# Kernel tuning notes

Hardware: AMD Instinct MI355X
Metric: run time of the kernel (lower is better)

The kernel has to match this reference:

```python
import jax, jax.numpy as jnp
import numpy as np

B, S, HID, NH = 2, 2048, 1024, 16
HD = HID // NH
BASE = 10000.0


def _rope_tables(seq_len, head_dim):
    i = jnp.arange(0, head_dim, 2, dtype=jnp.float32)
    theta = BASE ** (-i / head_dim)
    pos = jnp.arange(seq_len, dtype=jnp.float32)
    m_theta = jnp.outer(pos, theta)  # [S, HD/2]
    cos = jnp.repeat(jnp.cos(m_theta), 2, axis=1)  # [S, HD]
    sin = jnp.repeat(jnp.sin(m_theta), 2, axis=1)
    return cos, sin


def _apply_rope(x, cos, sin):
    # x: [B, NH, S, HD]; interleaved rotation: (-x1, x0, -x3, x2, ...)
    x_even = x[..., 0::2]
    x_odd = x[..., 1::2]
    inv_x = jnp.stack((-x_odd, x_even), axis=-1).reshape(x.shape)
    return x * cos[None, None] + inv_x * sin[None, None]


def setup_inputs() -> dict:
    key = jax.random.key(0)
    ks = jax.random.split(key, 7)
    q = jax.random.normal(ks[0], (B, S, HID), dtype=jnp.float32)
    k = jax.random.normal(ks[1], (B, S, HID), dtype=jnp.float32)
    v = jax.random.normal(ks[2], (B, S, HID), dtype=jnp.float32)
    scale = 1.0 / np.sqrt(HID)
    Wq = jax.random.normal(ks[3], (HID, HID), dtype=jnp.float32) * scale
    Wk = jax.random.normal(ks[4], (HID, HID), dtype=jnp.float32) * scale
    Wv = jax.random.normal(ks[5], (HID, HID), dtype=jnp.float32) * scale
    Wo = jax.random.normal(ks[6], (HID, HID), dtype=jnp.float32) * scale
    mask = jnp.triu(jnp.ones((S, S), dtype=bool), k=1)[None, None]  # causal, True = masked
    return {"q": q, "k": k, "v": v, "mask": mask,
            "Wq": Wq, "Wk": Wk, "Wv": Wv, "Wo": Wo}


def reference(q, k, v, mask, Wq, Wk, Wv, Wo):
    cos, sin = _rope_tables(S, HD)
    # Linear (torch stores weight as [out, in]; y = x @ W.T)
    qh = (q @ Wq.T).reshape(B, S, NH, HD).transpose(0, 2, 1, 3)
    kh = (k @ Wk.T).reshape(B, S, NH, HD).transpose(0, 2, 1, 3)
    vh = (v @ Wv.T).reshape(B, S, NH, HD).transpose(0, 2, 1, 3)
    qh = _apply_rope(qh, cos, sin)
    kh = _apply_rope(kh, cos, sin)
    scores = jnp.einsum("bhqd,bhkd->bhqk", qh, kh) / np.sqrt(HD)
    neg_min = jnp.finfo(jnp.float32).min
    scores = jnp.where(mask, neg_min, scores)
    attn = jax.nn.softmax(scores, axis=-1)
    out = jnp.einsum("bhqk,bhkd->bhqd", attn, vh)  # [B,NH,S,HD]
    out = out.transpose(0, 2, 1, 3).reshape(B, S, HID)
    return out @ Wo.T
```

## Files before the change

### kernel.cpp

```cpp
#include <hip/hip_runtime.h>

#define S_LEN 2048
#define HIDN  1024
#define NHEAD 16
#define HDIM  64
#define MROWS 4096
#define KDIM  1024
#define NDIM  1024

typedef __attribute__((ext_vector_type(8))) short bf16x8;
typedef __attribute__((ext_vector_type(4))) float f32x4;

static __device__ __forceinline__ ushort f2bf(float f) {
    unsigned int u = __float_as_uint(f);
    u = (u + 0x7fffu + ((u >> 16) & 1u)) >> 16;
    return (ushort)u;
}

static __device__ __forceinline__ void gload16(const ushort* g, ushort* l) {
    __builtin_amdgcn_global_load_lds(
        (const __attribute__((address_space(1))) unsigned int*)g,
        (__attribute__((address_space(3))) unsigned int*)l, 16, 0, 0);
}

__global__ __launch_bounds__(256) void prep_kernel(
    const float* __restrict__ q, const float* __restrict__ k,
    const float* __restrict__ v, const float* __restrict__ Wq,
    const float* __restrict__ Wk, const float* __restrict__ Wv,
    const float* __restrict__ Wo,
    ushort* __restrict__ qb, ushort* __restrict__ kb, ushort* __restrict__ vb,
    ushort* __restrict__ Wqb, ushort* __restrict__ Wkb, ushort* __restrict__ Wvb,
    ushort* __restrict__ Wob,
    float* __restrict__ rc, float* __restrict__ rs)
{
    const long Q4 = (long)MROWS * KDIM / 4;
    const long W4 = (long)NDIM * KDIM / 4;
    if (blockIdx.x < 16384) {
        long i = (long)blockIdx.x * 256 + threadIdx.x;
        const float* src; ushort* dst; long off;
        if (i < Q4)          { src = q; dst = qb; off = i; }
        else if (i < 2 * Q4) { src = k; dst = kb; off = i - Q4; }
        else if (i < 3 * Q4) { src = v; dst = vb; off = i - 2 * Q4; }
        else {
            long t = i - 3 * Q4;
            int wsel = (int)(t >> 18);
            off = t & (W4 - 1);
            src = (wsel == 0) ? Wq : (wsel == 1) ? Wk : (wsel == 2) ? Wv : Wo;
            dst = (wsel == 0) ? Wqb : (wsel == 1) ? Wkb : (wsel == 2) ? Wvb : Wob;
        }
        float4 vv = ((const float4*)src)[off];
        ushort4 o;
        o.x = f2bf(vv.x); o.y = f2bf(vv.y); o.z = f2bf(vv.z); o.w = f2bf(vv.w);
        ((ushort4*)dst)[off] = o;
    } else {
        int idx = (blockIdx.x - 16384) * 256 + threadIdx.x;
        int s  = idx >> 5;
        int jp = idx & 31;
        float theta = expf(-(float)(2 * jp) * (9.210340371976184f / 64.0f));
        float ang = (float)s * theta;
        float sv, cv;
        sincosf(ang, &sv, &cv);
        rc[idx] = cv;
        rs[idx] = sv;
    }
}

static __device__ __forceinline__ void gemm_mainloop(
    const ushort* __restrict__ A, const ushort* __restrict__ W,
    ushort* As, ushort* Bs, f32x4 (&acc)[2][4],
    int m0, int n0, int tid)
{
    const int lane = tid & 63, wid = tid >> 6;
    const int wm = wid & 1, wn = wid >> 1;
    const int quad = lane >> 4, l15 = lane & 15;

    for (int k0 = 0; k0 < KDIM; k0 += 64) {
        __syncthreads();
#pragma unroll
        for (int rr = 0; rr < 2; ++rr) {
            int sidx = tid + rr * 256;
            int row = sidx >> 3;
            int g = (sidx & 7) ^ (row & 7);
            gload16(A + (size_t)(m0 + row) * KDIM + k0 + g * 8, As + sidx * 8);
        }
#pragma unroll
        for (int rr = 0; rr < 4; ++rr) {
            int sidx = tid + rr * 256;
            int row = sidx >> 3;
            int g = (sidx & 7) ^ (row & 7);
            gload16(W + (size_t)(n0 + row) * KDIM + k0 + g * 8, Bs + sidx * 8);
        }
        __syncthreads();

#pragma unroll
        for (int ks = 0; ks < 2; ++ks) {
            bf16x8 af[2], bfr[4];
#pragma unroll
            for (int i = 0; i < 2; ++i) {
                int row = wm * 32 + i * 16 + l15;
                int gg = ((ks << 2) | quad) ^ (row & 7);
                af[i] = *(const bf16x8*)&As[row * 64 + gg * 8];
            }
#pragma unroll
            for (int j = 0; j < 4; ++j) {
                int row = wn * 64 + j * 16 + l15;
                int gg = ((ks << 2) | quad) ^ (row & 7);
                bfr[j] = *(const bf16x8*)&Bs[row * 64 + gg * 8];
            }
#pragma unroll
            for (int i = 0; i < 2; ++i)
#pragma unroll
                for (int j = 0; j < 4; ++j)
                    acc[i][j] = __builtin_amdgcn_mfma_f32_16x16x32_bf16(
                        af[i], bfr[j], acc[i][j], 0, 0, 0);
        }
    }
}

__global__ __launch_bounds__(256) void gemm_qkv(
    const ushort* __restrict__ qb, const ushort* __restrict__ kb,
    const ushort* __restrict__ vb,
    const ushort* __restrict__ Wqb, const ushort* __restrict__ Wkb,
    const ushort* __restrict__ Wvb,
    ushort* __restrict__ Qh, ushort* __restrict__ Kh, ushort* __restrict__ Vt,
    const float* __restrict__ rc, const float* __restrict__ rs)
{
    __shared__ __align__(16) ushort As[64 * 64];
    __shared__ __align__(16) ushort Bs[128 * 64];

    const int tid = threadIdx.x;
    const int lane = tid & 63, wid = tid >> 6;
    const int wm = wid & 1, wn = wid >> 1;
    const int quad = lane >> 4, l15 = lane & 15;
    const int z = blockIdx.z;

    const ushort* A; const ushort* W; int m0, n0;
    if (z == 2) {
        int flat = blockIdx.y * 8 + blockIdx.x;
        m0 = (flat >> 5) * 64;
        n0 = (flat & 31) * 128;
        A = Wvb; W = vb;
    } else {
        m0 = blockIdx.y * 64; n0 = blockIdx.x * 128;
        A = (z == 0) ? qb : kb;
        W = (z == 0) ? Wqb : Wkb;
    }

    f32x4 acc[2][4];
#pragma unroll
    for (int i = 0; i < 2; ++i)
#pragma unroll
        for (int j = 0; j < 4; ++j) acc[i][j] = 0.0f;

    gemm_mainloop(A, W, As, Bs, acc, m0, n0, tid);

    if (z != 2) {
        ushort* out = (z == 0) ? Qh : Kh;
        const float scale = (z == 0) ? 0.18033688011112042f : 1.0f;
#pragma unroll
        for (int i = 0; i < 2; ++i)
#pragma unroll
            for (int j = 0; j < 4; ++j)
#pragma unroll
                for (int r = 0; r < 4; ++r) {
                    int m = m0 + wm * 32 + i * 16 + quad * 4 + r;
                    int n = n0 + wn * 64 + j * 16 + l15;
                    float v = acc[i][j][r];
                    int b = m >> 11, s = m & (S_LEN - 1);
                    int h = n >> 6, d = n & 63;
                    int pidx = s * 32 + (d >> 1);
                    float cv = rc[pidx], sv = rs[pidx];
                    float partner = __shfl_xor(v, 1);
                    v = (d & 1) ? (v * cv + partner * sv)
                                : (v * cv - partner * sv);
                    out[((size_t)((b * NHEAD + h) * S_LEN + s)) * HDIM + d] =
                        f2bf(v * scale);
                }
    } else {
#pragma unroll
        for (int i = 0; i < 2; ++i)
#pragma unroll
            for (int j = 0; j < 4; ++j)
#pragma unroll
                for (int r = 0; r < 4; ++r) {
                    int m = m0 + wm * 32 + i * 16 + quad * 4 + r;
                    int n = n0 + wn * 64 + j * 16 + l15;
                    int h = m >> 6, d = m & 63;
                    int b = n >> 11, s = n & (S_LEN - 1);
                    Vt[((size_t)((b * NHEAD + h) * HDIM + d)) * S_LEN + s] =
                        f2bf(acc[i][j][r]);
                }
    }
}

__global__ __launch_bounds__(256) void gemm_out(
    const ushort* __restrict__ A, const ushort* __restrict__ W,
    float* __restrict__ out)
{
    __shared__ __align__(16) ushort As[64 * 64];
    __shared__ __align__(16) ushort Bs[128 * 64];

    const int tid = threadIdx.x;
    const int lane = tid & 63, wid = tid >> 6;
    const int wm = wid & 1, wn = wid >> 1;
    const int quad = lane >> 4, l15 = lane & 15;
    const int m0 = blockIdx.y * 64, n0 = blockIdx.x * 128;

    f32x4 acc[2][4];
#pragma unroll
    for (int i = 0; i < 2; ++i)
#pragma unroll
        for (int j = 0; j < 4; ++j) acc[i][j] = 0.0f;

    gemm_mainloop(A, W, As, Bs, acc, m0, n0, tid);

#pragma unroll
    for (int i = 0; i < 2; ++i)
#pragma unroll
        for (int j = 0; j < 4; ++j)
#pragma unroll
            for (int r = 0; r < 4; ++r) {
                int m = m0 + wm * 32 + i * 16 + quad * 4 + r;
                int n = n0 + wn * 64 + j * 16 + l15;
                out[(size_t)m * NDIM + n] = acc[i][j][r];
            }
}

__global__ __launch_bounds__(256) void attn_mfma(
    const ushort* __restrict__ Qh, const ushort* __restrict__ Kh,
    const ushort* __restrict__ Vt, ushort* __restrict__ AO)
{
    __shared__ __align__(16) ushort Ks[64 * 64];
    __shared__ __align__(16) ushort Vs[64 * 64];
    __shared__ __align__(16) ushort Ps[64 * 72];

    const int tid = threadIdx.x;
    const int lane = tid & 63, w = tid >> 6;
    const int quad = lane >> 4, l15 = lane & 15;
    const int id = blockIdx.x;
    const int b = id >> 9, h = (id >> 5) & 15, xr = id & 31;
    const int qt = b ? (31 - xr) : xr;
    const int q0 = qt * 64;
    const size_t hoff = (size_t)(b * NHEAD + h) * S_LEN * HDIM;

    bf16x8 qf[2];
#pragma unroll
    for (int ks = 0; ks < 2; ++ks)
        qf[ks] = *(const bf16x8*)(Qh + hoff +
            (size_t)(q0 + w * 16 + l15) * HDIM + ks * 32 + quad * 8);

    bf16x8 ones;
#pragma unroll
    for (int i = 0; i < 8; ++i) ones[i] = (short)0x3F80;

    f32x4 Oa[4];
    f32x4 Lacc = 0.0f;
#pragma unroll
    for (int j = 0; j < 4; ++j) Oa[j] = 0.0f;

    const int rowq = q0 + w * 16 + quad * 4;

    for (int kt = 0; kt <= qt; ++kt) {
        const int k0 = kt * 64;
        const bool diag = (kt == qt);
        __syncthreads();
#pragma unroll
        for (int rr = 0; rr < 2; ++rr) {
            int sidx = tid + rr * 256;
            int row = sidx >> 3;
            int g = (sidx & 7) ^ (row & 7);
            gload16(Kh + hoff + (size_t)(k0 + row) * HDIM + g * 8, Ks + sidx * 8);
            gload16(Vt + hoff + (size_t)row * S_LEN + k0 + g * 8, Vs + sidx * 8);
        }
        __syncthreads();

        f32x4 Sa[4];
#pragma unroll
        for (int j = 0; j < 4; ++j) Sa[j] = 0.0f;
#pragma unroll
        for (int ks = 0; ks < 2; ++ks) {
            const int p = ((ks << 2) | quad) ^ (l15 & 7);
            bf16x8 kf[4];
#pragma unroll
            for (int j = 0; j < 4; ++j)
                kf[j] = *(const bf16x8*)&Ks[(j * 16 + l15) * 64 + p * 8];
#pragma unroll
            for (int j = 0; j < 4; ++j)
                Sa[j] = __builtin_amdgcn_mfma_f32_16x16x32_bf16(qf[ks], kf[j],
                                                                Sa[j], 0, 0, 0);
        }

#pragma unroll
        for (int j = 0; j < 4; ++j) {
#pragma unroll
            for (int r = 0; r < 4; ++r) {
                float p = exp2f(Sa[j][r]);
                if (diag) {
                    int key = k0 + j * 16 + l15;
                    if (key > rowq + r) p = 0.f;
                }
                Ps[(w * 16 + quad * 4 + r) * 72 + j * 16 + l15] =
                    (ushort)(__float_as_uint(p) >> 16);
            }
        }

#pragma unroll
        for (int ks = 0; ks < 2; ++ks) {
            const int p = ((ks << 2) | quad) ^ (l15 & 7);
            bf16x8 pf = *(const bf16x8*)&Ps[(w * 16 + l15) * 72 + ks * 32 + quad * 8];
            bf16x8 vf[4];
#pragma unroll
            for (int j = 0; j < 4; ++j)
                vf[j] = *(const bf16x8*)&Vs[(j * 16 + l15) * 64 + p * 8];
#pragma unroll
            for (int j = 0; j < 4; ++j)
                Oa[j] = __builtin_amdgcn_mfma_f32_16x16x32_bf16(pf, vf[j],
                                                                Oa[j], 0, 0, 0);
            Lacc = __builtin_amdgcn_mfma_f32_16x16x32_bf16(pf, ones, Lacc, 0, 0, 0);
        }
    }

#pragma unroll
    for (int r = 0; r < 4; ++r) {
        float inv = 1.0f / Lacc[r];
        int srow = rowq + r;
#pragma unroll
        for (int j = 0; j < 4; ++j) {
            int d = j * 16 + l15;
            AO[((size_t)(b * S_LEN + srow)) * HIDN + h * HDIM + d] =
                f2bf(Oa[j][r] * inv);
        }
    }
}

extern "C" void kernel_launch(void* const* d_in, const int* in_sizes, int n_in,
                              void* d_out, int out_size, void* d_ws, size_t ws_size,
                              hipStream_t stream) {
    const float* qf  = (const float*)d_in[0];
    const float* kf  = (const float*)d_in[1];
    const float* vf  = (const float*)d_in[2];
    const float* Wqf = (const float*)d_in[4];
    const float* Wkf = (const float*)d_in[5];
    const float* Wvf = (const float*)d_in[6];
    const float* Wof = (const float*)d_in[7];
    float* out = (float*)d_out;

    char* wsp = (char*)d_ws;
    float* rc = (float*)wsp;            wsp += 65536 * 4;
    float* rs = (float*)wsp;            wsp += 65536 * 4;
    ushort* qb  = (ushort*)wsp;         wsp += (size_t)MROWS * KDIM * 2;
    ushort* kb  = (ushort*)wsp;         wsp += (size_t)MROWS * KDIM * 2;
    ushort* vb  = (ushort*)wsp;         wsp += (size_t)MROWS * KDIM * 2;
    ushort* Wqb = (ushort*)wsp;         wsp += (size_t)NDIM * KDIM * 2;
    ushort* Wkb = (ushort*)wsp;         wsp += (size_t)NDIM * KDIM * 2;
    ushort* Wvb = (ushort*)wsp;         wsp += (size_t)NDIM * KDIM * 2;
    ushort* Wob = (ushort*)wsp;         wsp += (size_t)NDIM * KDIM * 2;
    ushort* Qh  = (ushort*)wsp;         wsp += (size_t)MROWS * HIDN * 2;
    ushort* Kh  = (ushort*)wsp;         wsp += (size_t)MROWS * HIDN * 2;
    ushort* Vt  = (ushort*)wsp;         wsp += (size_t)MROWS * HIDN * 2;
    ushort* AO  = (ushort*)wsp;

    prep_kernel<<<16640, 256, 0, stream>>>(qf, kf, vf, Wqf, Wkf, Wvf, Wof,
                                           qb, kb, vb, Wqb, Wkb, Wvb, Wob, rc, rs);

    gemm_qkv<<<dim3(8, 64, 3), 256, 0, stream>>>(
        qb, kb, vb, Wqb, Wkb, Wvb, Qh, Kh, Vt, rc, rs);

    attn_mfma<<<1024, 256, 0, stream>>>(Qh, Kh, Vt, AO);

    gemm_out<<<dim3(8, 64), 256, 0, stream>>>(AO, Wob, out);
}
```

Baseline: 225.8 us.

## Split causal attention across blocks for load balance and add combine kernel

```diff
diff --git a/kernel.cpp b/kernel.cpp
--- a/kernel.cpp
+++ b/kernel.cpp
@@ -15,6 +15,9 @@
     unsigned int u = __float_as_uint(f);
     u = (u + 0x7fffu + ((u >> 16) & 1u)) >> 16;
     return (ushort)u;
+}
+static __device__ __forceinline__ float bf2f(ushort u) {
+    return __uint_as_float(((unsigned int)u) << 16);
 }
 
 static __device__ __forceinline__ void gload16(const ushort* g, ushort* l) {
@@ -136,12 +139,11 @@
 
     const ushort* A; const ushort* W; int m0, n0;
     if (z == 2) {
-        int flat = blockIdx.y * 8 + blockIdx.x;
-        m0 = (flat >> 5) * 64;
-        n0 = (flat & 31) * 128;
+        m0 = ((int)blockIdx.y * 2 + ((int)blockIdx.x >> 5)) * 64;
+        n0 = ((int)blockIdx.x & 31) * 128;
         A = Wvb; W = vb;
     } else {
-        m0 = blockIdx.y * 64; n0 = blockIdx.x * 128;
+        m0 = blockIdx.x * 64; n0 = blockIdx.y * 128;
         A = (z == 0) ? qb : kb;
         W = (z == 0) ? Wqb : Wkb;
     }
@@ -204,7 +206,7 @@
     const int lane = tid & 63, wid = tid >> 6;
     const int wm = wid & 1, wn = wid >> 1;
     const int quad = lane >> 4, l15 = lane & 15;
-    const int m0 = blockIdx.y * 64, n0 = blockIdx.x * 128;
+    const int m0 = blockIdx.x * 64, n0 = blockIdx.y * 128;
 
     f32x4 acc[2][4];
 #pragma unroll
@@ -228,7 +230,9 @@
 
 __global__ __launch_bounds__(256) void attn_mfma(
     const ushort* __restrict__ Qh, const ushort* __restrict__ Kh,
-    const ushort* __restrict__ Vt, ushort* __restrict__ AO)
+    const ushort* __restrict__ Vt,
+    ushort* __restrict__ O0, ushort* __restrict__ O1,
+    float* __restrict__ L0, float* __restrict__ L1)
 {
     __shared__ __align__(16) ushort Ks[64 * 64];
     __shared__ __align__(16) ushort Vs[64 * 64];
@@ -238,99 +242,125 @@
     const int lane = tid & 63, w = tid >> 6;
     const int quad = lane >> 4, l15 = lane & 15;
     const int id = blockIdx.x;
-    const int b = id >> 9, h = (id >> 5) & 15, xr = id & 31;
-    const int qt = b ? (31 - xr) : xr;
-    const int q0 = qt * 64;
+    const int h = id & 15, y = (id >> 4) & 31, b = id >> 9;
     const size_t hoff = (size_t)(b * NHEAD + h) * S_LEN * HDIM;
 
-    bf16x8 qf[2];
-#pragma unroll
-    for (int ks = 0; ks < 2; ++ks)
-        qf[ks] = *(const bf16x8*)(Qh + hoff +
-            (size_t)(q0 + w * 16 + l15) * HDIM + ks * 32 + quad * 8);
-
     bf16x8 ones;
 #pragma unroll
     for (int i = 0; i < 8; ++i) ones[i] = (short)0x3F80;
 
-    f32x4 Oa[4];
-    f32x4 Lacc = 0.0f;
-#pragma unroll
-    for (int j = 0; j < 4; ++j) Oa[j] = 0.0f;
-
-    const int rowq = q0 + w * 16 + quad * 4;
-
-    for (int kt = 0; kt <= qt; ++kt) {
-        const int k0 = kt * 64;
-        const bool diag = (kt == qt);
-        __syncthreads();
-#pragma unroll
-        for (int rr = 0; rr < 2; ++rr) {
-            int sidx = tid + rr * 256;
-            int row = sidx >> 3;
-            int g = (sidx & 7) ^ (row & 7);
-            gload16(Kh + hoff + (size_t)(k0 + row) * HDIM + g * 8, Ks + sidx * 8);
-            gload16(Vt + hoff + (size_t)row * S_LEN + k0 + g * 8, Vs + sidx * 8);
-        }
-        __syncthreads();
-
-        f32x4 Sa[4];
-#pragma unroll
-        for (int j = 0; j < 4; ++j) Sa[j] = 0.0f;
-#pragma unroll
-        for (int ks = 0; ks < 2; ++ks) {
-            const int p = ((ks << 2) | quad) ^ (l15 & 7);
-            bf16x8 kf[4];
+#pragma unroll
+    for (int seg = 0; seg < 2; ++seg) {
+        const int qt = seg ? (31 - y) : y;
+        const int lo = seg ? ((33 - y) >> 1) : 0;
+        const int hi = seg ? (32 - y) : ((y + 2) >> 1);
+        const int q0 = qt * 64;
+
+        bf16x8 qf[2];
+#pragma unroll
+        for (int ks = 0; ks < 2; ++ks)
+            qf[ks] = *(const bf16x8*)(Qh + hoff +
+                (size_t)(q0 + w * 16 + l15) * HDIM + ks * 32 + quad * 8);
+
+        f32x4 Oa[4];
+        f32x4 Lacc = 0.0f;
+#pragma unroll
+        for (int j = 0; j < 4; ++j) Oa[j] = 0.0f;
+
+        const int rowq = q0 + w * 16 + quad * 4;
+
+        for (int kt = lo; kt < hi; ++kt) {
+            const int k0 = kt * 64;
+            const bool diag = (kt == qt);
+            __syncthreads();
+#pragma unroll
+            for (int rr = 0; rr < 2; ++rr) {
+                int sidx = tid + rr * 256;
+                int row = sidx >> 3;
+                int g = (sidx & 7) ^ (row & 7);
+                gload16(Kh + hoff + (size_t)(k0 + row) * HDIM + g * 8, Ks + sidx * 8);
+                gload16(Vt + hoff + (size_t)row * S_LEN + k0 + g * 8, Vs + sidx * 8);
+            }
+            __syncthreads();
+
+            f32x4 Sa[4];
+#pragma unroll
+            for (int j = 0; j < 4; ++j) Sa[j] = 0.0f;
+#pragma unroll
+            for (int ks = 0; ks < 2; ++ks) {
+                const int p = ((ks << 2) | quad) ^ (l15 & 7);
+                bf16x8 kf[4];
+#pragma unroll
+                for (int j = 0; j < 4; ++j)
+                    kf[j] = *(const bf16x8*)&Ks[(j * 16 + l15) * 64 + p * 8];
+#pragma unroll
+                for (int j = 0; j < 4; ++j)
+                    Sa[j] = __builtin_amdgcn_mfma_f32_16x16x32_bf16(qf[ks], kf[j],
+                                                                    Sa[j], 0, 0, 0);
+            }
+
+#pragma unroll
+            for (int j = 0; j < 4; ++j) {
+#pragma unroll
+                for (int r = 0; r < 4; ++r) {
+                    float p = exp2f(Sa[j][r]);
+                    if (diag) {
+                        int key = k0 + j * 16 + l15;
+                        if (key > rowq + r) p = 0.f;
+                    }
+                    Ps[(w * 16 + quad * 4 + r) * 72 + j * 16 + l15] =
+                        (ushort)(__float_as_uint(p) >> 16);
+                }
+            }
+
+#pragma unroll
+            for (int ks = 0; ks < 2; ++ks) {
+                const int p = ((ks << 2) | quad) ^ (l15 & 7);
+                bf16x8 pf = *(const bf16x8*)&Ps[(w * 16 + l15) * 72 + ks * 32 + quad * 8];
+                bf16x8 vf[4];
+#pragma unroll
+                for (int j = 0; j < 4; ++j)
+                    vf[j] = *(const bf16x8*)&Vs[(j * 16 + l15) * 64 + p * 8];
+#pragma unroll
+                for (int j = 0; j < 4; ++j)
+                    Oa[j] = __builtin_amdgcn_mfma_f32_16x16x32_bf16(pf, vf[j],
+                                                                    Oa[j], 0, 0, 0);
+                Lacc = __builtin_amdgcn_mfma_f32_16x16x32_bf16(pf, ones, Lacc, 0, 0, 0);
+            }
+        }
+
+        ushort* Op = seg ? O1 : O0;
+        float*  Lp = seg ? L1 : L0;
+        const size_t rbase = ((size_t)(b * NHEAD + h) * S_LEN + rowq);
+#pragma unroll
+        for (int r = 0; r < 4; ++r) {
 #pragma unroll
             for (int j = 0; j < 4; ++j)
-                kf[j] = *(const bf16x8*)&Ks[(j * 16 + l15) * 64 + p * 8];
-#pragma unroll
-            for (int j = 0; j < 4; ++j)
-                Sa[j] = __builtin_amdgcn_mfma_f32_16x16x32_bf16(qf[ks], kf[j],
-                                                                Sa[j], 0, 0, 0);
-        }
-
-#pragma unroll
-        for (int j = 0; j < 4; ++j) {
-#pragma unroll
-            for (int r = 0; r < 4; ++r) {
-                float p = exp2f(Sa[j][r]);
-                if (diag) {
-                    int key = k0 + j * 16 + l15;
-                    if (key > rowq + r) p = 0.f;
-                }
-                Ps[(w * 16 + quad * 4 + r) * 72 + j * 16 + l15] =
-                    (ushort)(__float_as_uint(p) >> 16);
-            }
-        }
-
-#pragma unroll
-        for (int ks = 0; ks < 2; ++ks) {
-            const int p = ((ks << 2) | quad) ^ (l15 & 7);
-            bf16x8 pf = *(const bf16x8*)&Ps[(w * 16 + l15) * 72 + ks * 32 + quad * 8];
-            bf16x8 vf[4];
-#pragma unroll
-            for (int j = 0; j < 4; ++j)
-                vf[j] = *(const bf16x8*)&Vs[(j * 16 + l15) * 64 + p * 8];
-#pragma unroll
-            for (int j = 0; j < 4; ++j)
-                Oa[j] = __builtin_amdgcn_mfma_f32_16x16x32_bf16(pf, vf[j],
-                                                                Oa[j], 0, 0, 0);
-            Lacc = __builtin_amdgcn_mfma_f32_16x16x32_bf16(pf, ones, Lacc, 0, 0, 0);
+                Op[(rbase + r) * HDIM + j * 16 + l15] = f2bf(Oa[j][r]);
+            if (l15 == 0) Lp[rbase + r] = Lacc[r];
         }
     }
-
-#pragma unroll
-    for (int r = 0; r < 4; ++r) {
-        float inv = 1.0f / Lacc[r];
-        int srow = rowq + r;
-#pragma unroll
-        for (int j = 0; j < 4; ++j) {
-            int d = j * 16 + l15;
-            AO[((size_t)(b * S_LEN + srow)) * HIDN + h * HDIM + d] =
-                f2bf(Oa[j][r] * inv);
-        }
-    }
+}
+
+__global__ __launch_bounds__(256) void combine_kernel(
+    const ushort* __restrict__ O0, const ushort* __restrict__ O1,
+    const float* __restrict__ L0, const float* __restrict__ L1,
+    ushort* __restrict__ AO)
+{
+    int flat = blockIdx.x * 256 + threadIdx.x;
+    int row = flat >> 4;
+    int dq = (flat & 15) * 4;
+    int bh = row >> 11, s = row & (S_LEN - 1);
+    int b = bh >> 4, h = bh & 15;
+    ushort4 a = *(const ushort4*)(O0 + (size_t)row * HDIM + dq);
+    ushort4 c = *(const ushort4*)(O1 + (size_t)row * HDIM + dq);
+    float inv = 1.0f / (L0[row] + L1[row]);
+    ushort4 o;
+    o.x = f2bf((bf2f(a.x) + bf2f(c.x)) * inv);
+    o.y = f2bf((bf2f(a.y) + bf2f(c.y)) * inv);
+    o.z = f2bf((bf2f(a.z) + bf2f(c.z)) * inv);
+    o.w = f2bf((bf2f(a.w) + bf2f(c.w)) * inv);
+    *(ushort4*)(AO + ((size_t)(b * S_LEN + s)) * HIDN + h * HDIM + dq) = o;
 }
 
 extern "C" void kernel_launch(void* const* d_in, const int* in_sizes, int n_in,
@@ -360,13 +390,20 @@
     ushort* Vt  = (ushort*)wsp;         wsp += (size_t)MROWS * HIDN * 2;
     ushort* AO  = (ushort*)wsp;
 
+    ushort* O0 = qb;
+    ushort* O1 = kb;
+    float*  L0 = (float*)vb;
+    float*  L1 = (float*)vb + 65536;
+
     prep_kernel<<<16640, 256, 0, stream>>>(qf, kf, vf, Wqf, Wkf, Wvf, Wof,
                                            qb, kb, vb, Wqb, Wkb, Wvb, Wob, rc, rs);
 
-    gemm_qkv<<<dim3(8, 64, 3), 256, 0, stream>>>(
+    gemm_qkv<<<dim3(64, 8, 3), 256, 0, stream>>>(
         qb, kb, vb, Wqb, Wkb, Wvb, Qh, Kh, Vt, rc, rs);
 
-    attn_mfma<<<1024, 256, 0, stream>>>(Qh, Kh, Vt, AO);
-
-    gemm_out<<<dim3(8, 64), 256, 0, stream>>>(AO, Wob, out);
-}
+    attn_mfma<<<1024, 256, 0, stream>>>(Qh, Kh, Vt, O0, O1, L0, L1);
+
+    combine_kernel<<<4096, 256, 0, stream>>>(O0, O1, L0, L1, AO);
+
+    gemm_out<<<dim3(64, 8), 256, 0, stream>>>(AO, Wob, out);
+}
```

After: 222.7 us. About the same (-1.4%).
